# Performance work log

Hardware: AMD Instinct MI355X
Metric: run time of the kernel (lower is better)

Reference implementation:

```python
import jax, jax.numpy as jnp
import numpy as np

CH = 512
RED = CH // 8  # 64


def setup_inputs() -> dict:
    key = jax.random.key(0)
    ks = jax.random.split(key, 8)
    s = 0.05
    x = jax.random.normal(ks[0], (4, CH, 64, 64), dtype=jnp.float32)
    Wq = jax.random.normal(ks[1], (RED, CH), dtype=jnp.float32) * s
    bq = jnp.zeros((RED,), dtype=jnp.float32)
    Wk = jax.random.normal(ks[2], (RED, CH), dtype=jnp.float32) * s
    bk = jnp.zeros((RED,), dtype=jnp.float32)
    Wv = jax.random.normal(ks[3], (CH, CH), dtype=jnp.float32) * s
    bv = jnp.zeros((CH,), dtype=jnp.float32)
    gamma = jnp.zeros((1,), dtype=jnp.float32)
    return {"x": x, "Wq": Wq, "bq": bq, "Wk": Wk, "bk": bk, "Wv": Wv, "bv": bv, "gamma": gamma}


def reference(x, Wq, bq, Wk, bk, Wv, bv, gamma):
    b, c, h, w = x.shape
    n = h * w
    xf = x.reshape(b, c, n)  # [b, c, n]
    # 1x1 convs == per-pixel linear over channels
    q = jnp.einsum('rc,bcn->bnr', Wq, xf) + bq[None, None, :]   # [b, n, red]
    k = jnp.einsum('rc,bcn->brn', Wk, xf) + bk[None, :, None]   # [b, red, n]
    v = jnp.einsum('oc,bcn->bon', Wv, xf) + bv[None, :, None]   # [b, c, n]
    energy = jnp.einsum('bnr,brm->bnm', q, k)                   # [b, n, n]
    attention = jax.nn.softmax(energy, axis=-1)
    # out[b,c,i] = sum_j v[b,c,j] * attention[b,i,j]
    out = jnp.einsum('bcj,bij->bci', v, attention).reshape(b, c, h, w)
    return gamma[0] * out + x
```

## Files before the change

### kernel.cpp

```cpp
#include <hip/hip_runtime.h>
#include <math.h>

#define CH 512
#define RED 64

typedef __attribute__((ext_vector_type(4))) float f32x4;
typedef long i64;

typedef const __attribute__((address_space(1))) void* gas_t;
typedef __attribute__((address_space(3))) void* las_t;

static __device__ __forceinline__ void gl16(const void* g, void* l) {
    __builtin_amdgcn_global_load_lds((gas_t)g, (las_t)l, 16, 0, 0);
}

static __device__ __forceinline__ unsigned pk4(float a, float b, float c, float d) {
    int w = __builtin_amdgcn_cvt_pk_fp8_f32(a, b, 0, false);
    w = __builtin_amdgcn_cvt_pk_fp8_f32(c, d, w, true);
    return (unsigned)w;
}
static __device__ __forceinline__ unsigned char pk1(float a) {
    return (unsigned char)(__builtin_amdgcn_cvt_pk_fp8_f32(a, a, 0, false) & 0xFF);
}

static __device__ __forceinline__ float fexp2(float v) {
#if __has_builtin(__builtin_amdgcn_exp2f)
    return __builtin_amdgcn_exp2f(v);
#else
    float r; asm("v_exp_f32 %0, %1" : "=v"(r) : "v"(v)); return r;
#endif
}

static __device__ __forceinline__ void barrier_raw() {
    asm volatile("" ::: "memory");
    __builtin_amdgcn_s_barrier();
    asm volatile("" ::: "memory");
}

__global__ __launch_bounds__(128) void prep_w(
    const float* __restrict__ Wq, const float* __restrict__ Wk,
    const float* __restrict__ Wv, unsigned char* __restrict__ Wcat)
{
    const int r = blockIdx.x, t = threadIdx.x;
    const float* src = (r < 64) ? (Wq + (size_t)r * CH)
                     : (r < 128) ? (Wk + (size_t)(r - 64) * CH)
                                 : (Wv + (size_t)(r - 128) * CH);
    const float4 v = *(const float4*)&src[t * 4];
    *(unsigned*)&Wcat[(size_t)r * CH + t * 4] = pk4(v.x, v.y, v.z, v.w);
}

__global__ __launch_bounds__(256) void cast_xt(
    const float* __restrict__ x, unsigned char* __restrict__ xT, int n)
{
    __shared__ float sX[64][65];
    const int b = blockIdx.z, i0 = blockIdx.x * 64, c0 = blockIdx.y * 64;
    const int t = threadIdx.x;
    #pragma unroll
    for (int s = 0; s < 4; ++s) {
        const int id = s * 256 + t, c = id >> 4, seg = id & 15;
        *(float4*)&sX[c][seg * 4] = *(const float4*)&x[((size_t)b * CH + c0 + c) * n + i0 + seg * 4];
    }
    __syncthreads();
    const int i = t >> 2, cp = t & 3;
    uint4 w;
    w.x = pk4(sX[cp*16+ 0][i], sX[cp*16+ 1][i], sX[cp*16+ 2][i], sX[cp*16+ 3][i]);
    w.y = pk4(sX[cp*16+ 4][i], sX[cp*16+ 5][i], sX[cp*16+ 6][i], sX[cp*16+ 7][i]);
    w.z = pk4(sX[cp*16+ 8][i], sX[cp*16+ 9][i], sX[cp*16+10][i], sX[cp*16+11][i]);
    w.w = pk4(sX[cp*16+12][i], sX[cp*16+13][i], sX[cp*16+14][i], sX[cp*16+15][i]);
    *(uint4*)&xT[((size_t)b * n + i0 + i) * CH + c0 + cp * 16] = w;
}

__global__ __launch_bounds__(256, 4) void qkv_gemm(
    const unsigned char* __restrict__ xT, const unsigned char* __restrict__ Wcat,
    const float* __restrict__ bq, const float* __restrict__ bk,
    const float* __restrict__ bv,
    unsigned char* __restrict__ qF, unsigned char* __restrict__ kF,
    unsigned char* __restrict__ v2, int n)
{
    __shared__ char smem[20480];
    const int b = blockIdx.z, i0 = blockIdx.x * 128, o0 = blockIdx.y * 128;
    const int t = threadIdx.x, lane = t & 63;
    const int quad = lane >> 4, l16 = lane & 15;
    const int wrow = (t >> 6) & 1, wcol = t >> 7;

    f32x4 acc[4][4];
    const f32x4 zz = {0.f, 0.f, 0.f, 0.f};
    #pragma unroll
    for (int mi = 0; mi < 4; ++mi)
        #pragma unroll
        for (int ci = 0; ci < 4; ++ci) acc[mi][ci] = zz;

    const unsigned char* Ab = xT + ((size_t)b * n + i0) * CH;
    const unsigned char* Bb = Wcat + (size_t)o0 * CH;

    for (int c0 = 0; c0 < CH; c0 += 64) {
        #pragma unroll
        for (int s = 0; s < 5; ++s) {
            const int c = s * 256 + t;
            const bool isA = c < 640;
            const int tc = isA ? c : c - 640;
            const int r = tc / 5, p = (tc % 5) & 3;
            gl16((isA ? Ab : Bb) + (size_t)r * CH + c0 + p * 16,
                 smem + (isA ? 0 : 10240) + (size_t)tc * 16);
        }
        __syncthreads();
        #pragma unroll
        for (int kk = 0; kk < 64; kk += 32) {
            i64 af[4], bf[4];
            #pragma unroll
            for (int mi = 0; mi < 4; ++mi)
                af[mi] = *(const i64*)(smem + (wrow * 64 + mi * 16 + l16) * 80 + kk + quad * 8);
            #pragma unroll
            for (int ci = 0; ci < 4; ++ci)
                bf[ci] = *(const i64*)(smem + 10240 + (wcol * 64 + ci * 16 + l16) * 80 + kk + quad * 8);
            #pragma unroll
            for (int mi = 0; mi < 4; ++mi)
                #pragma unroll
                for (int ci = 0; ci < 4; ++ci)
                    acc[mi][ci] = __builtin_amdgcn_mfma_f32_16x16x32_fp8_fp8(af[mi], bf[ci], acc[mi][ci], 0, 0, 0);
        }
        __syncthreads();
    }

    float bb[4], scl[4];
    #pragma unroll
    for (int ci = 0; ci < 4; ++ci) {
        const int o = wcol * 64 + ci * 16 + l16;
        if (o0 == 0) {
            bb[ci]  = (o < 64) ? bq[o] : bk[o - 64];
            scl[ci] = (o < 64) ? 1.44269504088896f : 1.0f;
        } else {
            bb[ci]  = bv[o0 - 128 + o];
            scl[ci] = 1.0f;
        }
    }
    __syncthreads();
    unsigned char* sE = (unsigned char*)smem;
    if (o0 == 0) {
        #pragma unroll
        for (int mi = 0; mi < 4; ++mi)
            #pragma unroll
            for (int ci = 0; ci < 4; ++ci)
                #pragma unroll
                for (int r = 0; r < 4; ++r)
                    sE[(wrow*64 + mi*16 + quad*4 + r) * 144 + wcol*64 + ci*16 + l16] =
                        pk1((acc[mi][ci][r] + bb[ci]) * scl[ci]);
    } else {
        #pragma unroll
        for (int mi = 0; mi < 4; ++mi)
            #pragma unroll
            for (int ci = 0; ci < 4; ++ci)
                #pragma unroll
                for (int r = 0; r < 4; ++r)
                    sE[(wcol*64 + ci*16 + l16) * 144 + wrow*64 + mi*16 + quad*4 + r] =
                        pk1(acc[mi][ci][r] + bb[ci]);
    }
    __syncthreads();
    if (o0 == 0) {
        #pragma unroll
        for (int u = 0; u < 2; ++u) {
            const int id = u * 256 + t, i = id >> 2, p = id & 3;
            *(uint4*)&qF[((size_t)b * n + i0 + i) * RED + p * 16] = *(const uint4*)&sE[i * 144 + p * 16];
        }
        #pragma unroll
        for (int u = 0; u < 2; ++u) {
            const int id = u * 256 + t, i = id >> 2, p = id & 3;
            *(uint4*)&kF[((size_t)b * n + i0 + i) * RED + p * 16] = *(const uint4*)&sE[i * 144 + 64 + p * 16];
        }
    } else {
        #pragma unroll
        for (int u = 0; u < 4; ++u) {
            const int id = u * 256 + t, o = id >> 3, p = id & 7;
            *(uint4*)&v2[((size_t)b * CH + (o0 - 128) + o) * n + i0 + p * 16] =
                *(const uint4*)&sE[o * 144 + p * 16];
        }
    }
}

__global__ __launch_bounds__(256, 4) void rowmax(
    const unsigned char* __restrict__ qF, const unsigned char* __restrict__ kF,
    unsigned* __restrict__ mKey, int n)
{
    __shared__ char smem[20480];
    const int b = blockIdx.z, i0 = blockIdx.y * 128, j0 = blockIdx.x * 128;
    const int t = threadIdx.x, lane = t & 63;
    const int quad = lane >> 4, l16 = lane & 15;
    const int wrow = (t >> 6) & 1, wcol = t >> 7;

    const unsigned char* Qb = qF + ((size_t)b * n + i0) * RED;
    const unsigned char* Kb = kF + ((size_t)b * n + j0) * RED;
    #pragma unroll
    for (int s = 0; s < 5; ++s) {
        const int c = s * 256 + t;
        const bool isQ = c < 640;
        const int tc = isQ ? c : c - 640;
        const int r = tc / 5, p = (tc % 5) & 3;
        gl16((isQ ? Qb : Kb) + (size_t)r * RED + p * 16,
             smem + (isQ ? 0 : 10240) + (size_t)tc * 16);
    }
    __syncthreads();

    f32x4 acc[4][4];
    const f32x4 zz = {0.f, 0.f, 0.f, 0.f};
    #pragma unroll
    for (int mi = 0; mi < 4; ++mi)
        #pragma unroll
        for (int ci = 0; ci < 4; ++ci) acc[mi][ci] = zz;

    #pragma unroll
    for (int kk = 0; kk < 64; kk += 32) {
        i64 af[4], bf[4];
        #pragma unroll
        for (int mi = 0; mi < 4; ++mi)
            af[mi] = *(const i64*)(smem + (wrow * 64 + mi * 16 + l16) * 80 + kk + quad * 8);
        #pragma unroll
        for (int ci = 0; ci < 4; ++ci)
            bf[ci] = *(const i64*)(smem + 10240 + (wcol * 64 + ci * 16 + l16) * 80 + kk + quad * 8);
        #pragma unroll
        for (int mi = 0; mi < 4; ++mi)
            #pragma unroll
            for (int ci = 0; ci < 4; ++ci)
                acc[mi][ci] = __builtin_amdgcn_mfma_f32_16x16x32_fp8_fp8(af[mi], bf[ci], acc[mi][ci], 0, 0, 0);
    }

    #pragma unroll
    for (int mi = 0; mi < 4; ++mi)
        #pragma unroll
        for (int r = 0; r < 4; ++r) {
            float mx = fmaxf(fmaxf(acc[mi][0][r], acc[mi][1][r]),
                             fmaxf(acc[mi][2][r], acc[mi][3][r]));
            #pragma unroll
            for (int off = 1; off < 16; off <<= 1) mx = fmaxf(mx, __shfl_xor(mx, off));
            if (l16 == 0) {
                union { float f; unsigned u; } cv; cv.f = mx;
                const unsigned key = ((int)cv.u >= 0) ? (cv.u + 0x80000000u) : ~cv.u;
                atomicMax(&mKey[(size_t)b * n + i0 + wrow * 64 + mi * 16 + quad * 4 + r], key);
            }
        }
}

#define STGSZ 20480
#define SPOFF 40960
#define SLOFF 45056

#define CHUNK(BASE, cc) do {                                                  \
    f32x4 S_[2] = {zz, zz};                                                   \
    __builtin_amdgcn_s_setprio(1);                                            \
    {                                                                         \
        const i64 kf0 = *(const i64*)(smem + (BASE) + fA);                    \
        const i64 kf1 = *(const i64*)(smem + (BASE) + (fA ^ 32));             \
        S_[0] = __builtin_amdgcn_mfma_f32_16x16x32_fp8_fp8(kf0, qreg[0][0], S_[0], 0, 0, 0); \
        S_[1] = __builtin_amdgcn_mfma_f32_16x16x32_fp8_fp8(kf0, qreg[1][0], S_[1], 0, 0, 0); \
        S_[0] = __builtin_amdgcn_mfma_f32_16x16x32_fp8_fp8(kf1, qreg[0][1], S_[0], 0, 0, 0); \
        S_[1] = __builtin_amdgcn_mfma_f32_16x16x32_fp8_fp8(kf1, qreg[1][1], S_[1], 0, 0, 0); \
    }                                                                         \
    __builtin_amdgcn_s_setprio(0);                                            \
    _Pragma("unroll")                                                         \
    for (int qt = 0; qt < 2; ++qt) {                                          \
        const float e0 = fexp2(S_[qt][0] - mrow[qt]);                         \
        const float e1 = fexp2(S_[qt][1] - mrow[qt]);                         \
        const float e2 = fexp2(S_[qt][2] - mrow[qt]);                         \
        const float e3 = fexp2(S_[qt][3] - mrow[qt]);                         \
        lacc[qt] += (e0 + e1) + (e2 + e3);                                    \
        *(unsigned*)(smem + pwA + qt * 1024) = pk4(e0, e1, e2, e3);           \
    }                                                                         \
    asm volatile("s_waitcnt lgkmcnt(0)" ::: "memory");                        \
    barrier_raw();         \
    __builtin_amdgcn_s_setprio(1);                                            \
    _Pragma("unroll")                                                         \
    for (int kki = 0; kki < 2; ++kki) {                                       \
        const int kx = kki << 5;                                              \
        i64 vf_[4], pf_[2];                                                   \
        _Pragma("unroll")                                                     \
        for (int ct = 0; ct < 4; ++ct)                                        \
            vf_[ct] = *(const i64*)(smem + (BASE) + (vA ^ kx) + ct * 1024);   \
        _Pragma("unroll")                                                     \
        for (int qt = 0; qt < 2; ++qt)                                        \
            pf_[qt] = *(const i64*)(smem + (pA ^ kx) + qt * 1024);            \
        _Pragma("unroll")                                                     \
        for (int qt = 0; qt < 2; ++qt)                                        \
            _Pragma("unroll")                                                 \
            for (int ct = 0; ct < 4; ++ct)                                    \
                acc[qt][ct] = __builtin_amdgcn_mfma_f32_16x16x32_fp8_fp8(vf_[ct], pf_[qt], acc[qt][ct], 0, 0, 0); \
    }                                                                         \
    __builtin_amdgcn_s_setprio(0);                                            \
    asm volatile("s_waitcnt lgkmcnt(0)" ::: "memory");                        \
    barrier_raw();                        \
    if ((cc) + 2 < nchunks) {                                                 \
        if (t < 256) gl16(kP, smem + (BASE) + kDstOff);                       \
        gl16(vP0, smem + (BASE) + vDstOff0);                                  \
        gl16(vP1, smem + (BASE) + vDstOff1);                                  \
        kP += 4096; vP0 += 64; vP1 += 64;                                     \
        if (w < 4) asm volatile("s_waitcnt vmcnt(3)" ::: "memory");           \
        else       asm volatile("s_waitcnt vmcnt(2)" ::: "memory");           \
        __builtin_amdgcn_sched_barrier(0);                                    \
        barrier_raw();                        \
    } else if ((cc) + 1 < nchunks) {                                          \
        asm volatile("s_waitcnt vmcnt(0)" ::: "memory");                      \
        __builtin_amdgcn_sched_barrier(0);                                    \
        barrier_raw();                                                        \
    }                                                                         \
} while (0)

__global__ __launch_bounds__(512, 4) void attn(
    const unsigned char* __restrict__ qF,
    const unsigned char* __restrict__ kF,
    const unsigned char* __restrict__ v2,
    const unsigned* __restrict__ mKey,
    const float* __restrict__ x, const float* __restrict__ gamma,
    float* __restrict__ y, int n)
{
    __shared__ char smem[46080];
    const int b = blockIdx.x >> 1, ch0 = (blockIdx.x & 1) * 256;
    const int i0 = blockIdx.y * 64;
    const int t = threadIdx.x, lane = t & 63, w = t >> 6;
    const int quad = lane >> 4, l16 = lane & 15;
    const int qh = w & 1, g = w >> 1;
    const int sw = (l16 >> 1) & 3;
    const int boff = (quad & 1) * 8;
    const int phalf = quad >> 1;
    const int p0 = phalf ^ sw;

    const int fA  = (g * 16 + l16) * 64 + p0 * 16 + boff;
    const int vA  = 4096 + (g * 64 + l16) * 64 + p0 * 16 + boff;
    const int pA  = SPOFF + (qh * 32 + l16) * 64 + p0 * 16 + boff;
    const int pwA = SPOFF + (qh * 32 + l16) * 64 + (g ^ sw) * 16 + quad * 4;

    const unsigned char* Qb = qF + ((size_t)b * n + i0) * RED;
    const unsigned char* Kb = kF + (size_t)b * n * RED;
    const unsigned char* Vb = v2 + ((size_t)b * CH + ch0) * n;

    const int r = t >> 2, s4 = t & 3, gs = s4 ^ ((r >> 1) & 3);
    const int kDstOff  = t * 16;
    const int vDstOff0 = 4096 + t * 16;
    const int vDstOff1 = 12288 + t * 16;
    const size_t vHalf = (size_t)128 * n;
    const unsigned char* kSrc0 = Kb + (size_t)r * RED + gs * 16;
    const unsigned char* vSrc0 = Vb + (size_t)r * n + gs * 16;

    if (t < 256) {
        gl16(Qb + (size_t)r * RED + gs * 16, smem + SPOFF + kDstOff);
        gl16(kSrc0, smem + kDstOff);
    }
    gl16(vSrc0, smem + vDstOff0);
    gl16(vSrc0 + vHalf, smem + vDstOff1);

    float mrow[2];
    #pragma unroll
    for (int qt = 0; qt < 2; ++qt) {
        const unsigned u = mKey[(size_t)b * n + i0 + qh * 32 + qt * 16 + l16];
        const unsigned bits = (u >= 0x80000000u) ? (u - 0x80000000u) : ~u;
        union { unsigned u; float f; } cv; cv.u = bits;
        mrow[qt] = cv.f;
    }
    __syncthreads();

    i64 qreg[2][2];
    #pragma unroll
    for (int qt = 0; qt < 2; ++qt) {
        #pragma unroll
        for (int kki = 0; kki < 2; ++kki)
            qreg[qt][kki] = *(const i64*)(smem + ((pA ^ (kki << 5)) + qt * 1024));
    }
    asm volatile("s_waitcnt lgkmcnt(0)" ::: "memory");
    barrier_raw();

    const int nchunks = n >> 6;
    if (nchunks > 1) {
        if (t < 256) gl16(kSrc0 + 4096, smem + STGSZ + kDstOff);
        gl16(vSrc0 + 64, smem + STGSZ + vDstOff0);
        gl16(vSrc0 + vHalf + 64, smem + STGSZ + vDstOff1);
    }
    const unsigned char* kP  = kSrc0 + 8192;
    const unsigned char* vP0 = vSrc0 + 128;
    const unsigned char* vP1 = vSrc0 + vHalf + 128;

    f32x4 acc[2][4];
    const f32x4 zz = {0.f, 0.f, 0.f, 0.f};
    #pragma unroll
    for (int qt = 0; qt < 2; ++qt)
        #pragma unroll
        for (int ct = 0; ct < 4; ++ct) acc[qt][ct] = zz;
    float lacc[2] = {0.f, 0.f};

    for (int c = 0; c < nchunks; c += 2) {
        CHUNK(0, c);
        CHUNK(STGSZ, c + 1);
    }

    float* sL = (float*)(smem + SLOFF);
    #pragma unroll
    for (int qt = 0; qt < 2; ++qt) {
        float v = lacc[qt];
        v += __shfl_xor(v, 16);
        v += __shfl_xor(v, 32);
        lacc[qt] = v;
    }
    if (quad == 0) {
        #pragma unroll
        for (int qt = 0; qt < 2; ++qt) sL[w * 32 + qt * 16 + l16] = lacc[qt];
    }
    __syncthreads();
    float il[2];
    #pragma unroll
    for (int qt = 0; qt < 2; ++qt) {
        const int idx = qt * 16 + l16;
        il[qt] = 1.0f / (sL[qh * 32 + idx] + sL[(2 + qh) * 32 + idx] +
                         sL[(4 + qh) * 32 + idx] + sL[(6 + qh) * 32 + idx]);
    }

    const float gm = gamma[0];
    float* sT = (float*)smem;
    #pragma unroll
    for (int cr = 0; cr < 4; ++cr) {
        __syncthreads();
        if (g == cr) {
            #pragma unroll
            for (int ct = 0; ct < 4; ++ct)
                #pragma unroll
                for (int qt = 0; qt < 2; ++qt)
                    #pragma unroll
                    for (int rr = 0; rr < 4; ++rr)
                        sT[(ct * 16 + quad * 4 + rr) * 68 + qh * 32 + qt * 16 + l16] =
                            acc[qt][ct][rr] * il[qt];
        }
        __syncthreads();
        const int row = t >> 3, seg = (t & 7) * 8;
        const size_t gb = ((size_t)b * CH + ch0 + cr * 64 + row) * n + i0 + seg;
        #pragma unroll
        for (int u = 0; u < 2; ++u) {
            const float4 xv = *(const float4*)&x[gb + u * 4];
            const float* op = &sT[row * 68 + seg + u * 4];
            float4 yv;
            yv.x = gm * op[0] + xv.x;
            yv.y = gm * op[1] + xv.y;
            yv.z = gm * op[2] + xv.z;
            yv.w = gm * op[3] + xv.w;
            *(float4*)&y[gb + u * 4] = yv;
        }
    }
}

extern "C" void kernel_launch(void* const* d_in, const int* in_sizes, int n_in,
                              void* d_out, int out_size, void* d_ws, size_t ws_size,
                              hipStream_t stream) {
    const float* x     = (const float*)d_in[0];
    const float* Wq    = (const float*)d_in[1];
    const float* bq    = (const float*)d_in[2];
    const float* Wk    = (const float*)d_in[3];
    const float* bk    = (const float*)d_in[4];
    const float* Wv    = (const float*)d_in[5];
    const float* bv    = (const float*)d_in[6];
    const float* gamma = (const float*)d_in[7];
    float* y = (float*)d_out;

    const int N = 64 * 64;
    const int B = in_sizes[0] / (CH * N);

    char* ws = (char*)d_ws;
    unsigned char* xT   = (unsigned char*)ws;  ws += (size_t)B * N * CH;
    unsigned char* qF   = (unsigned char*)ws;  ws += (size_t)B * N * RED;
    unsigned char* kF   = (unsigned char*)ws;  ws += (size_t)B * N * RED;
    unsigned char* v2   = (unsigned char*)ws;  ws += (size_t)B * CH * N;
    unsigned char* Wcat = (unsigned char*)ws;  ws += (size_t)640 * CH;
    unsigned* mKey      = (unsigned*)ws;

    hipMemsetAsync(mKey, 0, (size_t)B * N * 4, stream);

    prep_w<<<dim3(640), 128, 0, stream>>>(Wq, Wk, Wv, Wcat);
    cast_xt<<<dim3(N / 64, CH / 64, B), 256, 0, stream>>>(x, xT, N);
    qkv_gemm<<<dim3(N / 128, 5, B), 256, 0, stream>>>(xT, Wcat, bq, bk, bv, qF, kF, v2, N);
    rowmax<<<dim3(N / 128, N / 128, B), 256, 0, stream>>>(qF, kF, mKey, N);
    attn<<<dim3(2 * B, N / 64), 512, 0, stream>>>(qF, kF, v2, mKey, x, gamma, y, N);
}
```

Measured before the change: 228.3 us.

## Replace separate row-max pass with online softmax inside attention kernel

Removes the rowmax kernel, which recomputed the full QK^T product in fp8 to find exact per-row maxima, together with its memset and atomics. The attention kernel now keeps a running maximum per query row. Each chunk combines partial maxima across warps through shared memory, then rescales the running sum and output accumulators by exp2(old-new). This drops a full extra QK pass, but adds an extra barrier per chunk, shared-memory traffic and 32 multiplies per chunk in the attention inner loop.

```diff
diff --git a/kernel.cpp b/kernel.cpp
--- a/kernel.cpp
+++ b/kernel.cpp
@@ -177,92 +177,56 @@
     }
 }
 
-__global__ __launch_bounds__(256, 4) void rowmax(
-    const unsigned char* __restrict__ qF, const unsigned char* __restrict__ kF,
-    unsigned* __restrict__ mKey, int n)
-{
-    __shared__ char smem[20480];
-    const int b = blockIdx.z, i0 = blockIdx.y * 128, j0 = blockIdx.x * 128;
-    const int t = threadIdx.x, lane = t & 63;
-    const int quad = lane >> 4, l16 = lane & 15;
-    const int wrow = (t >> 6) & 1, wcol = t >> 7;
-
-    const unsigned char* Qb = qF + ((size_t)b * n + i0) * RED;
-    const unsigned char* Kb = kF + ((size_t)b * n + j0) * RED;
-    #pragma unroll
-    for (int s = 0; s < 5; ++s) {
-        const int c = s * 256 + t;
-        const bool isQ = c < 640;
-        const int tc = isQ ? c : c - 640;
-        const int r = tc / 5, p = (tc % 5) & 3;
-        gl16((isQ ? Qb : Kb) + (size_t)r * RED + p * 16,
-             smem + (isQ ? 0 : 10240) + (size_t)tc * 16);
-    }
-    __syncthreads();
-
-    f32x4 acc[4][4];
-    const f32x4 zz = {0.f, 0.f, 0.f, 0.f};
-    #pragma unroll
-    for (int mi = 0; mi < 4; ++mi)
-        #pragma unroll
-        for (int ci = 0; ci < 4; ++ci) acc[mi][ci] = zz;
-
-    #pragma unroll
-    for (int kk = 0; kk < 64; kk += 32) {
-        i64 af[4], bf[4];
-        #pragma unroll
-        for (int mi = 0; mi < 4; ++mi)
-            af[mi] = *(const i64*)(smem + (wrow * 64 + mi * 16 + l16) * 80 + kk + quad * 8);
-        #pragma unroll
-        for (int ci = 0; ci < 4; ++ci)
-            bf[ci] = *(const i64*)(smem + 10240 + (wcol * 64 + ci * 16 + l16) * 80 + kk + quad * 8);
-        #pragma unroll
-        for (int mi = 0; mi < 4; ++mi)
-            #pragma unroll
-            for (int ci = 0; ci < 4; ++ci)
-                acc[mi][ci] = __builtin_amdgcn_mfma_f32_16x16x32_fp8_fp8(af[mi], bf[ci], acc[mi][ci], 0, 0, 0);
-    }
-
-    #pragma unroll
-    for (int mi = 0; mi < 4; ++mi)
-        #pragma unroll
-        for (int r = 0; r < 4; ++r) {
-            float mx = fmaxf(fmaxf(acc[mi][0][r], acc[mi][1][r]),
-                             fmaxf(acc[mi][2][r], acc[mi][3][r]));
-            #pragma unroll
-            for (int off = 1; off < 16; off <<= 1) mx = fmaxf(mx, __shfl_xor(mx, off));
-            if (l16 == 0) {
-                union { float f; unsigned u; } cv; cv.f = mx;
-                const unsigned key = ((int)cv.u >= 0) ? (cv.u + 0x80000000u) : ~cv.u;
-                atomicMax(&mKey[(size_t)b * n + i0 + wrow * 64 + mi * 16 + quad * 4 + r], key);
-            }
-        }
-}
-
 #define STGSZ 20480
 #define SPOFF 40960
 #define SLOFF 45056
 
 #define CHUNK(BASE, cc) do {                                                  \
-    f32x4 S_[2] = {zz, zz};                                                   \
+    f32x4 S0 = zz, S1 = zz;                                                   \
     __builtin_amdgcn_s_setprio(1);                                            \
     {                                                                         \
         const i64 kf0 = *(const i64*)(smem + (BASE) + fA);                    \
         const i64 kf1 = *(const i64*)(smem + (BASE) + (fA ^ 32));             \
-        S_[0] = __builtin_amdgcn_mfma_f32_16x16x32_fp8_fp8(kf0, qreg[0][0], S_[0], 0, 0, 0); \
-        S_[1] = __builtin_amdgcn_mfma_f32_16x16x32_fp8_fp8(kf0, qreg[1][0], S_[1], 0, 0, 0); \
-        S_[0] = __builtin_amdgcn_mfma_f32_16x16x32_fp8_fp8(kf1, qreg[0][1], S_[0], 0, 0, 0); \
-        S_[1] = __builtin_amdgcn_mfma_f32_16x16x32_fp8_fp8(kf1, qreg[1][1], S_[1], 0, 0, 0); \
+        S0 = __builtin_amdgcn_mfma_f32_16x16x32_fp8_fp8(kf0, qreg[0][0], S0, 0, 0, 0); \
+        S1 = __builtin_amdgcn_mfma_f32_16x16x32_fp8_fp8(kf0, qreg[1][0], S1, 0, 0, 0); \
+        S0 = __builtin_amdgcn_mfma_f32_16x16x32_fp8_fp8(kf1, qreg[0][1], S0, 0, 0, 0); \
+        S1 = __builtin_amdgcn_mfma_f32_16x16x32_fp8_fp8(kf1, qreg[1][1], S1, 0, 0, 0); \
     }                                                                         \
     __builtin_amdgcn_s_setprio(0);                                            \
-    _Pragma("unroll")                                                         \
-    for (int qt = 0; qt < 2; ++qt) {                                          \
-        const float e0 = fexp2(S_[qt][0] - mrow[qt]);                         \
-        const float e1 = fexp2(S_[qt][1] - mrow[qt]);                         \
-        const float e2 = fexp2(S_[qt][2] - mrow[qt]);                         \
-        const float e3 = fexp2(S_[qt][3] - mrow[qt]);                         \
-        lacc[qt] += (e0 + e1) + (e2 + e3);                                    \
-        *(unsigned*)(smem + pwA + qt * 1024) = pk4(e0, e1, e2, e3);           \
+      \
+    float c0 = fmaxf(fmaxf(S0[0], S0[1]), fmaxf(S0[2], S0[3]));               \
+    float c1 = fmaxf(fmaxf(S1[0], S1[1]), fmaxf(S1[2], S1[3]));               \
+    c0 = fmaxf(c0, __shfl_xor(c0, 16)); c0 = fmaxf(c0, __shfl_xor(c0, 32));   \
+    c1 = fmaxf(c1, __shfl_xor(c1, 16)); c1 = fmaxf(c1, __shfl_xor(c1, 32));   \
+    if (quad == 0) {                                                          \
+        *(float*)(smem + mxW) = c0;                                           \
+        *(float*)(smem + mxW + 256) = c1;                                     \
+    }                                                                         \
+    asm volatile("s_waitcnt lgkmcnt(0)" ::: "memory");                        \
+    barrier_raw();                          \
+    {                                                                         \
+        const f32x4 mx0 = *(const f32x4*)(smem + mxR);                        \
+        const f32x4 mx1 = *(const f32x4*)(smem + mxR + 256);                  \
+        const float cd0 = fmaxf(fmaxf(mx0[0], mx0[1]), fmaxf(mx0[2], mx0[3]));\
+        const float cd1 = fmaxf(fmaxf(mx1[0], mx1[1]), fmaxf(mx1[2], mx1[3]));\
+        const float mn0 = fmaxf(mold[0], cd0), mn1 = fmaxf(mold[1], cd1);     \
+        const float rs0 = fexp2(mold[0] - mn0), rs1 = fexp2(mold[1] - mn1);   \
+        mold[0] = mn0; mold[1] = mn1;                                         \
+        const float e00 = fexp2(S0[0] - mn0), e01 = fexp2(S0[1] - mn0);       \
+        const float e02 = fexp2(S0[2] - mn0), e03 = fexp2(S0[3] - mn0);       \
+        lacc[0] = lacc[0] * rs0 + ((e00 + e01) + (e02 + e03));                \
+        *(unsigned*)(smem + pwA) = pk4(e00, e01, e02, e03);                   \
+        const float e10 = fexp2(S1[0] - mn1), e11 = fexp2(S1[1] - mn1);       \
+        const float e12 = fexp2(S1[2] - mn1), e13 = fexp2(S1[3] - mn1);       \
+        lacc[1] = lacc[1] * rs1 + ((e10 + e11) + (e12 + e13));                \
+        *(unsigned*)(smem + pwA + 1024) = pk4(e10, e11, e12, e13);            \
+        _Pragma("unroll")                                                     \
+        for (int ct = 0; ct < 4; ++ct)                                        \
+            _Pragma("unroll")                                                 \
+            for (int rr = 0; rr < 4; ++rr) {                                  \
+                acc[0][ct][rr] *= rs0;                                        \
+                acc[1][ct][rr] *= rs1;                                        \
+            }                                                                 \
     }                                                                         \
     asm volatile("s_waitcnt lgkmcnt(0)" ::: "memory");                        \
     barrier_raw();         \
@@ -285,7 +249,7 @@
     }                                                                         \
     __builtin_amdgcn_s_setprio(0);                                            \
     asm volatile("s_waitcnt lgkmcnt(0)" ::: "memory");                        \
-    barrier_raw();                        \
+    barrier_raw();                    \
     if ((cc) + 2 < nchunks) {                                                 \
         if (t < 256) gl16(kP, smem + (BASE) + kDstOff);                       \
         gl16(vP0, smem + (BASE) + vDstOff0);                                  \
@@ -294,7 +258,7 @@
         if (w < 4) asm volatile("s_waitcnt vmcnt(3)" ::: "memory");           \
         else       asm volatile("s_waitcnt vmcnt(2)" ::: "memory");           \
         __builtin_amdgcn_sched_barrier(0);                                    \
-        barrier_raw();                        \
+        barrier_raw();                    \
     } else if ((cc) + 1 < nchunks) {                                          \
         asm volatile("s_waitcnt vmcnt(0)" ::: "memory");                      \
         __builtin_amdgcn_sched_barrier(0);                                    \
@@ -306,7 +270,6 @@
     const unsigned char* __restrict__ qF,
     const unsigned char* __restrict__ kF,
     const unsigned char* __restrict__ v2,
-    const unsigned* __restrict__ mKey,
     const float* __restrict__ x, const float* __restrict__ gamma,
     float* __restrict__ y, int n)
 {
@@ -325,6 +288,8 @@
     const int vA  = 4096 + (g * 64 + l16) * 64 + p0 * 16 + boff;
     const int pA  = SPOFF + (qh * 32 + l16) * 64 + p0 * 16 + boff;
     const int pwA = SPOFF + (qh * 32 + l16) * 64 + (g ^ sw) * 16 + quad * 4;
+    const int mxR = SLOFF + qh * 512 + l16 * 16;
+    const int mxW = mxR + g * 4;
 
     const unsigned char* Qb = qF + ((size_t)b * n + i0) * RED;
     const unsigned char* Kb = kF + (size_t)b * n * RED;
@@ -344,15 +309,6 @@
     }
     gl16(vSrc0, smem + vDstOff0);
     gl16(vSrc0 + vHalf, smem + vDstOff1);
-
-    float mrow[2];
-    #pragma unroll
-    for (int qt = 0; qt < 2; ++qt) {
-        const unsigned u = mKey[(size_t)b * n + i0 + qh * 32 + qt * 16 + l16];
-        const unsigned bits = (u >= 0x80000000u) ? (u - 0x80000000u) : ~u;
-        union { unsigned u; float f; } cv; cv.u = bits;
-        mrow[qt] = cv.f;
-    }
     __syncthreads();
 
     i64 qreg[2][2];
@@ -382,6 +338,7 @@
         #pragma unroll
         for (int ct = 0; ct < 4; ++ct) acc[qt][ct] = zz;
     float lacc[2] = {0.f, 0.f};
+    float mold[2] = {-3.0e38f, -3.0e38f};
 
     for (int c = 0; c < nchunks; c += 2) {
         CHUNK(0, c);
@@ -396,6 +353,7 @@
         v += __shfl_xor(v, 32);
         lacc[qt] = v;
     }
+    __syncthreads();
     if (quad == 0) {
         #pragma unroll
         for (int qt = 0; qt < 2; ++qt) sL[w * 32 + qt * 16 + l16] = lacc[qt];
@@ -462,14 +420,10 @@
     unsigned char* qF   = (unsigned char*)ws;  ws += (size_t)B * N * RED;
     unsigned char* kF   = (unsigned char*)ws;  ws += (size_t)B * N * RED;
     unsigned char* v2   = (unsigned char*)ws;  ws += (size_t)B * CH * N;
-    unsigned char* Wcat = (unsigned char*)ws;  ws += (size_t)640 * CH;
-    unsigned* mKey      = (unsigned*)ws;
-
-    hipMemsetAsync(mKey, 0, (size_t)B * N * 4, stream);
+    unsigned char* Wcat = (unsigned char*)ws;
 
     prep_w<<<dim3(640), 128, 0, stream>>>(Wq, Wk, Wv, Wcat);
     cast_xt<<<dim3(N / 64, CH / 64, B), 256, 0, stream>>>(x, xT, N);
     qkv_gemm<<<dim3(N / 128, 5, B), 256, 0, stream>>>(xT, Wcat, bq, bk, bv, qF, kF, v2, N);
-    rowmax<<<dim3(N / 128, N / 128, B), 256, 0, stream>>>(qF, kF, mKey, N);
-    attn<<<dim3(2 * B, N / 64), 512, 0, stream>>>(qF, kF, v2, mKey, x, gamma, y, N);
-}
+    attn<<<dim3(2 * B, N / 64), 512, 0, stream>>>(qF, kF, v2, x, gamma, y, N);
+}
```

Result: no change. 227.5 us (-0.3%).
